# Optimization experiments

Hardware: AMD Instinct MI355X
Metric: run time of the kernel (lower is better)

Reference implementation:

```python
import math
import jax, jax.numpy as jnp
import numpy as np

VOCAB = 80; MAX_SEQ_LEN = 32; D_MODEL = 512; NHEAD = 8; DFF = 2048; NLAYERS = 6
EOS = 1; SOS = 2; PAD = 0; BATCH = 8; MEM_LEN = 256; PE_LEN = MAX_SEQ_LEN + 2
EPS = 1e-5


def _sinusoid(max_len, d):
    pos = np.arange(max_len)[:, None].astype(np.float32)
    div = np.exp(np.arange(0, d, 2).astype(np.float32) * -(math.log(10000.0) / d))
    pe = np.zeros((max_len, d), np.float32)
    pe[:, 0::2] = np.sin(pos * div)
    pe[:, 1::2] = np.cos(pos * div)
    return jnp.asarray(pe)


def setup_inputs() -> dict:
    key = jax.random.key(0)
    ks = jax.random.split(key, 10)
    s = 0.02
    def n(k, shape, scale=s):
        return jax.random.normal(k, shape, jnp.float32) * scale
    return {
        "memory": n(ks[0], (BATCH, MEM_LEN, D_MODEL), 1.0),
        "emb_table": n(ks[1], (VOCAB, D_MODEL), 1.0),
        "pe": _sinusoid(PE_LEN, D_MODEL),
        "sa_in_w": n(ks[2], (NLAYERS, 3 * D_MODEL, D_MODEL)),
        "sa_in_b": jnp.zeros((NLAYERS, 3 * D_MODEL), jnp.float32),
        "sa_out_w": n(ks[3], (NLAYERS, D_MODEL, D_MODEL)),
        "sa_out_b": jnp.zeros((NLAYERS, D_MODEL), jnp.float32),
        "ca_in_w": n(ks[4], (NLAYERS, 3 * D_MODEL, D_MODEL)),
        "ca_in_b": jnp.zeros((NLAYERS, 3 * D_MODEL), jnp.float32),
        "ca_out_w": n(ks[5], (NLAYERS, D_MODEL, D_MODEL)),
        "ca_out_b": jnp.zeros((NLAYERS, D_MODEL), jnp.float32),
        "ln_w": jnp.ones((NLAYERS, 3, D_MODEL), jnp.float32),
        "ln_b": jnp.zeros((NLAYERS, 3, D_MODEL), jnp.float32),
        "ff1_w": n(ks[6], (NLAYERS, DFF, D_MODEL)),
        "ff1_b": jnp.zeros((NLAYERS, DFF), jnp.float32),
        "ff2_w": n(ks[7], (NLAYERS, D_MODEL, DFF)),
        "ff2_b": jnp.zeros((NLAYERS, D_MODEL), jnp.float32),
        "clf_w": n(ks[8], (VOCAB, D_MODEL)),
        "clf_b": jnp.zeros((VOCAB,), jnp.float32),
    }


def _layer_norm(x, g, b):
    mu = jnp.mean(x, -1, keepdims=True)
    var = jnp.mean((x - mu) ** 2, -1, keepdims=True)
    return (x - mu) * jax.lax.rsqrt(var + EPS) * g + b


def _mha(q_in, kv_in, in_w, in_b, out_w, out_b, mask):
    d = q_in.shape[-1]; hd = d // NHEAD
    wq, wk, wv = jnp.split(in_w, 3, 0)
    bq, bk, bv = jnp.split(in_b, 3)
    B, Tq, _ = q_in.shape; Tk = kv_in.shape[1]
    q = (q_in @ wq.T + bq).reshape(B, Tq, NHEAD, hd)
    k = (kv_in @ wk.T + bk).reshape(B, Tk, NHEAD, hd)
    v = (kv_in @ wv.T + bv).reshape(B, Tk, NHEAD, hd)
    scores = jnp.einsum('bqhd,bkhd->bhqk', q, k) / math.sqrt(hd)
    if mask is not None:
        scores = jnp.where(mask, -1e9, scores)
    probs = jax.nn.softmax(scores, -1)
    out = jnp.einsum('bhqk,bkhd->bqhd', probs, v).reshape(B, Tq, d)
    return out @ out_w.T + out_b


def _decoder(tgt, memory, causal, p):
    # post-norm TransformerDecoder (torch default, dropout=identity at inference)
    x = tgt
    for l in range(NLAYERS):
        x = _layer_norm(x + _mha(x, x, p['sa_in_w'][l], p['sa_in_b'][l], p['sa_out_w'][l], p['sa_out_b'][l], causal), p['ln_w'][l, 0], p['ln_b'][l, 0])
        x = _layer_norm(x + _mha(x, memory, p['ca_in_w'][l], p['ca_in_b'][l], p['ca_out_w'][l], p['ca_out_b'][l], None), p['ln_w'][l, 1], p['ln_b'][l, 1])
        h = jax.nn.gelu(x @ p['ff1_w'][l].T + p['ff1_b'][l], approximate=False)
        x = _layer_norm(x + h @ p['ff2_w'][l].T + p['ff2_b'][l], p['ln_w'][l, 2], p['ln_b'][l, 2])
    return x


def _greedy(memory, emb_table, pe, p, clf_w, clf_b):
    B = memory.shape[0]; T1 = MAX_SEQ_LEN + 1
    sq = math.sqrt(D_MODEL)
    causal = jnp.triu(jnp.ones((T1, T1), bool), 1)[None, None]  # True = blocked
    tgt0 = jnp.zeros((B, T1, D_MODEL), memory.dtype)
    tgt0 = tgt0.at[:, 0].set(pe[0] + emb_table[SOS] * sq)

    def step(tgt, t):
        # full recompute of the whole decoder stack each step (no KV cache),
        # causal mask makes position t depend only on the valid prefix.
        out = _decoder(tgt, memory, causal, p)
        out_t = jax.lax.dynamic_slice_in_dim(out, t, 1, 1)[:, 0]
        logits = out_t @ clf_w.T + clf_b
        pred = jnp.argmax(logits, -1)
        # original uses pe[len(sampled_ids)] == pe[t+2] for the token at slot t+1
        new_e = jnp.take(pe, t + 2, axis=0) + emb_table[pred] * sq
        tgt = jax.lax.dynamic_update_slice_in_dim(tgt, new_e[:, None, :], t + 1, 1)
        return tgt, (logits, pred)

    _, (logits, preds) = jax.lax.scan(step, tgt0, jnp.arange(MAX_SEQ_LEN))
    all_logits = jnp.transpose(logits, (1, 0, 2))  # [B, T, V]
    sampled = jnp.concatenate([jnp.full((B, 1), SOS, preds.dtype), preds.T], 1)
    eos_idx = jnp.argmax(sampled == EOS, 1)  # first eos (0 if none, as torch)
    sampled = jnp.where(jnp.arange(T1)[None] <= eos_idx[:, None], PAD, sampled)
    return all_logits, sampled


def reference(memory, emb_table, pe, sa_in_w, sa_in_b, sa_out_w, sa_out_b, ca_in_w, ca_in_b, ca_out_w, ca_out_b, ln_w, ln_b, ff1_w, ff1_b, ff2_w, ff2_b, clf_w, clf_b):
    p = dict(sa_in_w=sa_in_w, sa_in_b=sa_in_b, sa_out_w=sa_out_w, sa_out_b=sa_out_b,
             ca_in_w=ca_in_w, ca_in_b=ca_in_b, ca_out_w=ca_out_w, ca_out_b=ca_out_b,
             ln_w=ln_w, ln_b=ln_b, ff1_w=ff1_w, ff1_b=ff1_b, ff2_w=ff2_w, ff2_b=ff2_b)
    return _greedy(memory, emb_table, pe, p, clf_w, clf_b)
```

## Files before the change

kernel.cpp:

```cpp
#include <hip/hip_runtime.h>
#include <math.h>

constexpr int T1 = 33, NL = 6, VOC = 80;
constexpr float SQD = 22.62741699796952f;

__device__ float g_memk[(size_t)NL * 2048 * 512];
__device__ float g_memv[(size_t)NL * 2048 * 512];
__device__ float g_kc[(size_t)NL * 8 * T1 * 512];
__device__ float g_vc[(size_t)NL * 8 * T1 * 512];
__device__ float g_x[8 * 512], g_x2[8 * 512], g_y[8 * 512], g_q[8 * 512], g_att[8 * 512];
__device__ float g_h[8 * 2048];
__device__ int   g_tok[8 * T1];

struct DecP {
  const float *mem, *emb, *pe, *saw, *sab, *sow, *sob, *caw, *cab, *cow, *cob,
              *lnw, *lnb, *f1w, *f1b, *f2w, *f2b, *cw, *cb;
  float* out;
};

__global__ __launch_bounds__(256) void k_memkv(const float* __restrict__ mem,
                                               const float* __restrict__ caw,
                                               const float* __restrict__ cab) {
  __shared__ float mlds[128][34];
  __shared__ float wlds[256][34];
  const int tid = threadIdx.x;
  const int l = blockIdx.x / 64, rem = blockIdx.x % 64;
  const int mt = rem >> 2, rt = rem & 3;
  const float* wbase = caw + (size_t)l * 1536 * 512 + (size_t)512 * 512;

  float acc[8][16];
#pragma unroll
  for (int i = 0; i < 8; ++i)
#pragma unroll
    for (int j = 0; j < 16; ++j) acc[i][j] = 0.f;

  const int tm = tid >> 4, tr = tid & 15;

  for (int kb = 0; kb < 16; ++kb) {
    __syncthreads();
    {
      int row = tid >> 1, half = tid & 1;
      const float2* src = (const float2*)(mem + (size_t)(mt * 128 + row) * 512 + kb * 32 + half * 16);
      float2* dst = (float2*)&mlds[row][half * 16];
#pragma unroll
      for (int q = 0; q < 8; ++q) dst[q] = src[q];
    }
    {
      int c2 = (tid & 15) * 2, rb = tid >> 4;
#pragma unroll
      for (int q = 0; q < 16; ++q) {
        int row = rb + 16 * q;
        *(float2*)&wlds[row][c2] =
            *(const float2*)(wbase + (size_t)(rt * 256 + row) * 512 + kb * 32 + c2);
      }
    }
    __syncthreads();
#pragma unroll 4
    for (int k2 = 0; k2 < 16; ++k2) {
      float2 mv[8];
#pragma unroll
      for (int i = 0; i < 8; ++i) mv[i] = *(const float2*)&mlds[tm * 8 + i][2 * k2];
#pragma unroll
      for (int j = 0; j < 16; ++j) {
        float2 w2 = *(const float2*)&wlds[tr + 16 * j][2 * k2];
#pragma unroll
        for (int i = 0; i < 8; ++i) acc[i][j] += mv[i].x * w2.x + mv[i].y * w2.y;
      }
    }
  }
#pragma unroll
  for (int i = 0; i < 8; ++i) {
    int mrow = mt * 128 + tm * 8 + i;
#pragma unroll
    for (int j = 0; j < 16; ++j) {
      int r = rt * 256 + tr + 16 * j;
      float v = acc[i][j] + cab[l * 1536 + 512 + r];
      if (r < 512) g_memk[((size_t)l * 2048 + mrow) * 512 + r] = v;
      else         g_memv[((size_t)l * 2048 + mrow) * 512 + (r - 512)] = v;
    }
  }
}

__device__ __forceinline__ float wave_reduce8(const float (&acc)[8], int lane) {
  float a0, a1, a2, a3;
  {
    bool hi = lane & 1;
    float s0 = hi ? acc[0] : acc[1], s1 = hi ? acc[2] : acc[3];
    float s2 = hi ? acc[4] : acc[5], s3 = hi ? acc[6] : acc[7];
    float r0 = __shfl_xor(s0, 1), r1 = __shfl_xor(s1, 1);
    float r2 = __shfl_xor(s2, 1), r3 = __shfl_xor(s3, 1);
    a0 = (hi ? acc[1] : acc[0]) + r0;  a1 = (hi ? acc[3] : acc[2]) + r1;
    a2 = (hi ? acc[5] : acc[4]) + r2;  a3 = (hi ? acc[7] : acc[6]) + r3;
  }
  float b0, b1;
  {
    bool hi = lane & 2;
    float s0 = hi ? a0 : a1, s1 = hi ? a2 : a3;
    float r0 = __shfl_xor(s0, 2), r1 = __shfl_xor(s1, 2);
    b0 = (hi ? a1 : a0) + r0;  b1 = (hi ? a3 : a2) + r1;
  }
  float f;
  {
    bool hi = lane & 4;
    float s = hi ? b0 : b1;
    float r = __shfl_xor(s, 4);
    f = (hi ? b1 : b0) + r;
  }
  f += __shfl_xor(f, 8);  f += __shfl_xor(f, 16);  f += __shfl_xor(f, 32);
  return f;
}

__device__ __forceinline__ void stage_in(float (*sx)[520], const float* __restrict__ g,
                                         bool doLN, const float* __restrict__ lw,
                                         const float* __restrict__ lb, float* __restrict__ wb) {
  const int tid = threadIdx.x;
#pragma unroll
  for (int q = 0; q < 4; ++q) {
    int f4 = tid + 256 * q;
    int b = f4 >> 7, c = (f4 & 127) << 2;
    float4 v = ((const float4*)g)[f4];
    *(float4*)&sx[b][c] = v;
  }
  __syncthreads();
  if (doLN) {
    const int lane = tid & 63, wv = tid >> 6;
#pragma unroll
    for (int rr = 0; rr < 2; ++rr) {
      int b = wv + 4 * rr;
      float vals[8]; float sm = 0.f;
#pragma unroll
      for (int j = 0; j < 8; ++j) { vals[j] = sx[b][lane + 64 * j]; sm += vals[j]; }
#pragma unroll
      for (int o = 32; o; o >>= 1) sm += __shfl_xor(sm, o);
      float mu = sm * (1.f / 512.f);
      float s2 = 0.f;
#pragma unroll
      for (int j = 0; j < 8; ++j) { float d = vals[j] - mu; s2 += d * d; }
#pragma unroll
      for (int o = 32; o; o >>= 1) s2 += __shfl_xor(s2, o);
      float rstd = 1.f / sqrtf(s2 * (1.f / 512.f) + 1e-5f);
#pragma unroll
      for (int j = 0; j < 8; ++j) {
        int c = lane + 64 * j;
        sx[b][c] = (vals[j] - mu) * rstd * lw[c] + lb[c];
      }
    }
    __syncthreads();
  }
  if (wb && blockIdx.x == 0) {
#pragma unroll
    for (int q = 0; q < 4; ++q) {
      int f4 = tid + 256 * q;
      int b = f4 >> 7, c = (f4 & 127) << 2;
      ((float4*)wb)[f4] = *(float4*)&sx[b][c];
    }
  }
}

template <int MODE>
__device__ __forceinline__ void gemv512(float (*sx)[520], const float* __restrict__ W,
                                        const float* __restrict__ bias, int rpb,
                                        float* __restrict__ out, const float* __restrict__ res,
                                        int l, int t) {
  const int lane = threadIdx.x & 63, wv = threadIdx.x >> 6;
  const int r0 = blockIdx.x * rpb;
  for (int rr = wv; rr < rpb; rr += 4) {
    const int r = r0 + rr;
    const float* wr = W + (size_t)r * 512;
    float acc[8] = {0, 0, 0, 0, 0, 0, 0, 0};
#pragma unroll
    for (int j = 0; j < 8; ++j) {
      float w = wr[lane + 64 * j];
#pragma unroll
      for (int b = 0; b < 8; ++b) acc[b] += w * sx[b][lane + 64 * j];
    }
    float f = wave_reduce8(acc, lane);
    if (lane < 8) {
      const int b = lane;
      float v = f + bias[r];
      if constexpr (MODE == 0) {
        if (r < 512)       out[b * 512 + r] = v;
        else if (r < 1024) g_kc[(((size_t)l * 8 + b) * T1 + t) * 512 + (r - 512)] = v;
        else               g_vc[(((size_t)l * 8 + b) * T1 + t) * 512 + (r - 1024)] = v;
      } else if constexpr (MODE == 1) {
        out[b * 512 + r] = v + res[b * 512 + r];
      } else if constexpr (MODE == 2) {
        out[b * 512 + r] = v;
      } else {
        out[b * 2048 + r] = 0.5f * v * (1.f + erff(v * 0.70710678118654752f));
      }
    }
  }
}

__device__ __forceinline__ void stage_h(float (*sb)[2052]) {
  const int tid = threadIdx.x;
#pragma unroll
  for (int q = 0; q < 16; ++q) {
    int f4 = tid + 256 * q;
    int b = f4 >> 9, c = (f4 & 511) << 2;
    *(float4*)&sb[b][c] = ((const float4*)g_h)[f4];
  }
}

__device__ __forceinline__ void gemvH(float (*sb)[2052], const float* __restrict__ W,
                                      const float* __restrict__ bias,
                                      const float* __restrict__ res, float* __restrict__ out) {
  const int lane = threadIdx.x & 63, wv = threadIdx.x >> 6;
  const int r0 = blockIdx.x * 8;
  for (int rr = wv; rr < 8; rr += 4) {
    const int r = r0 + rr;
    const float* wr = W + (size_t)r * 2048;
    float acc[8] = {0, 0, 0, 0, 0, 0, 0, 0};
#pragma unroll 8
    for (int j = 0; j < 32; ++j) {
      float w = wr[lane + 64 * j];
#pragma unroll
      for (int b = 0; b < 8; ++b) acc[b] += w * sb[b][lane + 64 * j];
    }
    float f = wave_reduce8(acc, lane);
    if (lane < 8) out[lane * 512 + r] = f + bias[r] + res[lane * 512 + r];
  }
}

__global__ __launch_bounds__(256) void k_start(DecP P) {
  int b = blockIdx.x;
#pragma unroll
  for (int q = 0; q < 2; ++q) {
    int c = threadIdx.x + 256 * q;
    g_x[b * 512 + c] = P.pe[c] + P.emb[2 * 512 + c] * SQD;
  }
  if (threadIdx.x == 0) g_tok[b * T1] = 2;
}

__global__ __launch_bounds__(256) void k_A(DecP P, int l, int t) {
  __shared__ float sx[8][520];
  const float* lw = (l > 0) ? P.lnw + ((l - 1) * 3 + 2) * 512 : P.lnw;
  const float* lb = (l > 0) ? P.lnb + ((l - 1) * 3 + 2) * 512 : P.lnb;
  stage_in(sx, (l == 0) ? g_x : g_y, l > 0, lw, lb, (l > 0) ? g_x : nullptr);
  gemv512<0>(sx, P.saw + (size_t)l * 1536 * 512, P.sab + l * 1536, 8, g_q, nullptr, l, t);
}

__global__ __launch_bounds__(64) void k_B(DecP P, int l, int t) {
  __shared__ float s_p[128];
  const int lane = threadIdx.x;
  const int b = blockIdx.x >> 3, h = blockIdx.x & 7;
  s_p[lane] = g_q[b * 512 + h * 64 + lane];
  asm volatile("s_waitcnt lgkmcnt(0)" ::: "memory");
  __builtin_amdgcn_sched_barrier(0);
  float sc = -3.4e38f;
  if (lane <= t) {
    const float4* kr = (const float4*)&g_kc[(((size_t)l * 8 + b) * T1 + lane) * 512 + h * 64];
    float s = 0.f;
#pragma unroll
    for (int d4 = 0; d4 < 16; ++d4) {
      float4 kv = kr[d4];
      s += s_p[d4 * 4 + 0] * kv.x + s_p[d4 * 4 + 1] * kv.y +
           s_p[d4 * 4 + 2] * kv.z + s_p[d4 * 4 + 3] * kv.w;
    }
    sc = s * 0.125f;
  }
  float m = sc;
#pragma unroll
  for (int o = 32; o; o >>= 1) m = fmaxf(m, __shfl_xor(m, o));
  float ex = (lane <= t) ? expf(sc - m) : 0.f;
  float sum = ex;
#pragma unroll
  for (int o = 32; o; o >>= 1) sum += __shfl_xor(sum, o);
  s_p[64 + lane] = ex / sum;
  asm volatile("s_waitcnt lgkmcnt(0)" ::: "memory");
  __builtin_amdgcn_sched_barrier(0);
  float o = 0.f;
  for (int j = 0; j <= t; ++j)
    o += s_p[64 + j] * g_vc[(((size_t)l * 8 + b) * T1 + j) * 512 + h * 64 + lane];
  g_att[b * 512 + h * 64 + lane] = o;
}

__global__ __launch_bounds__(256) void k_C(DecP P, int l) {
  __shared__ float sx[8][520];
  stage_in(sx, g_att, false, nullptr, nullptr, nullptr);
  gemv512<1>(sx, P.sow + (size_t)l * 512 * 512, P.sob + l * 512, 8, g_y, g_x, l, 0);
}

__global__ __launch_bounds__(256) void k_D(DecP P, int l) {
  __shared__ float sx[8][520];
  stage_in(sx, g_y, true, P.lnw + (l * 3 + 0) * 512, P.lnb + (l * 3 + 0) * 512, g_x2);
  gemv512<2>(sx, P.caw + (size_t)l * 1536 * 512, P.cab + l * 1536, 8, g_q, nullptr, l, 0);
}

__global__ __launch_bounds__(256) void k_E(DecP P, int l) {
  __shared__ float s_p[336];
  __shared__ float s_w[4][2];
  __shared__ float s_pv[4][64];
  const int tid = threadIdx.x;
  const int lane = tid & 63, wv = tid >> 6;
  const int b = blockIdx.x >> 3, h = blockIdx.x & 7;
  if (tid < 64) s_p[tid] = g_q[b * 512 + h * 64 + tid];
  __syncthreads();
  int m0 = wv * 64 + lane;
  const float4* kr = (const float4*)&g_memk[((size_t)l * 2048 + b * 256 + m0) * 512 + h * 64];
  float s = 0.f;
#pragma unroll
  for (int d4 = 0; d4 < 16; ++d4) {
    float4 kv = kr[d4];
    s += s_p[d4 * 4 + 0] * kv.x + s_p[d4 * 4 + 1] * kv.y +
         s_p[d4 * 4 + 2] * kv.z + s_p[d4 * 4 + 3] * kv.w;
  }
  s *= 0.125f;
  float m = s;
#pragma unroll
  for (int o = 32; o; o >>= 1) m = fmaxf(m, __shfl_xor(m, o));
  if (lane == 0) s_w[wv][0] = m;
  __syncthreads();
  float M = fmaxf(fmaxf(s_w[0][0], s_w[1][0]), fmaxf(s_w[2][0], s_w[3][0]));
  float ex = expf(s - M);
  float sum = ex;
#pragma unroll
  for (int o = 32; o; o >>= 1) sum += __shfl_xor(sum, o);
  if (lane == 0) s_w[wv][1] = sum;
  __syncthreads();
  float S = s_w[0][1] + s_w[1][1] + s_w[2][1] + s_w[3][1];
  s_p[64 + m0] = ex / S;
  __syncthreads();
  float o = 0.f;
  const float* vbase = &g_memv[((size_t)l * 2048 + b * 256) * 512 + h * 64];
  for (int j = 0; j < 64; ++j) {
    int mm = wv * 64 + j;
    o += s_p[64 + mm] * vbase[(size_t)mm * 512 + lane];
  }
  s_pv[wv][lane] = o;
  __syncthreads();
  if (wv == 0) {
    float tot = s_pv[0][lane] + s_pv[1][lane] + s_pv[2][lane] + s_pv[3][lane];
    g_att[b * 512 + h * 64 + lane] = tot;
  }
}

__global__ __launch_bounds__(256) void k_F(DecP P, int l) {
  __shared__ float sx[8][520];
  stage_in(sx, g_att, false, nullptr, nullptr, nullptr);
  gemv512<1>(sx, P.cow + (size_t)l * 512 * 512, P.cob + l * 512, 8, g_y, g_x2, l, 0);
}

__global__ __launch_bounds__(256) void k_G(DecP P, int l) {
  __shared__ float sx[8][520];
  stage_in(sx, g_y, true, P.lnw + (l * 3 + 1) * 512, P.lnb + (l * 3 + 1) * 512, g_x2);
  gemv512<3>(sx, P.f1w + (size_t)l * 2048 * 512, P.f1b + l * 2048, 8, g_h, nullptr, l, 0);
}

__global__ __launch_bounds__(256) void k_H(DecP P, int l) {
  __shared__ float sb[8][2052];
  stage_h(sb);
  __syncthreads();
  gemvH(sb, P.f2w + (size_t)l * 512 * 2048, P.f2b + l * 512, g_x2, g_y);
}

__global__ __launch_bounds__(256) void k_T(DecP P, int t) {
  __shared__ float sx[8][520];
  __shared__ float s_p[80];
  __shared__ int s_int[1];
  const int tid = threadIdx.x;
  const int lane = tid & 63, wv = tid >> 6;
  const int b = blockIdx.x;
  stage_in(sx, g_y, true, P.lnw + (5 * 3 + 2) * 512, P.lnb + (5 * 3 + 2) * 512, nullptr);
  for (int i = 0; i < 20; ++i) {
    int r = wv * 20 + i;
    const float* wr = P.cw + (size_t)r * 512;
    float a = 0.f;
#pragma unroll
    for (int j = 0; j < 8; ++j) a += wr[lane + 64 * j] * sx[b][lane + 64 * j];
#pragma unroll
    for (int o = 32; o; o >>= 1) a += __shfl_xor(a, o);
    if (lane == 0) {
      float v = a + P.cb[r];
      s_p[r] = v;
      P.out[((size_t)b * 32 + t) * VOC + r] = v;
    }
  }
  __syncthreads();
  if (wv == 0) {
    float v1 = s_p[lane];
    int i1 = lane;
    if (lane < 16) {
      float v2 = s_p[64 + lane];
      if (v2 > v1) { v1 = v2; i1 = 64 + lane; }
    }
#pragma unroll
    for (int o = 32; o; o >>= 1) {
      float ov = __shfl_xor(v1, o);
      int oi = __shfl_xor(i1, o);
      if (ov > v1 || (ov == v1 && oi < i1)) { v1 = ov; i1 = oi; }
    }
    if (lane == 0) { s_int[0] = i1; g_tok[b * T1 + t + 1] = i1; }
  }
  __syncthreads();
  int pred = s_int[0];
#pragma unroll
  for (int q = 0; q < 2; ++q) {
    int c = tid + 256 * q;
    g_x[b * 512 + c] = P.pe[(t + 2) * 512 + c] + P.emb[(size_t)pred * 512 + c] * SQD;
  }
}

__global__ __launch_bounds__(64) void k_out(DecP P) {
  int lane = threadIdx.x;
  if (lane < 8) {
    int b = lane;
    int eos = -1;
    for (int j = 0; j < T1; ++j) {
      int tk = g_tok[b * T1 + j];
      if (tk == 1 && eos < 0) eos = j;
    }
    if (eos < 0) eos = 0;
    for (int j = 0; j < T1; ++j) {
      int tk = g_tok[b * T1 + j];
      P.out[20480 + b * T1 + j] = (j <= eos) ? 0.f : (float)tk;
    }
  }
}

extern "C" void kernel_launch(void* const* d_in, const int* in_sizes, int n_in,
                              void* d_out, int out_size, void* d_ws, size_t ws_size,
                              hipStream_t stream) {
  (void)in_sizes; (void)n_in; (void)d_ws; (void)ws_size; (void)out_size;
  const float* mem = (const float*)d_in[0];
  const float* emb = (const float*)d_in[1];
  const float* pe  = (const float*)d_in[2];
  const float* saw = (const float*)d_in[3];
  const float* sab = (const float*)d_in[4];
  const float* sow = (const float*)d_in[5];
  const float* sob = (const float*)d_in[6];
  const float* caw = (const float*)d_in[7];
  const float* cab = (const float*)d_in[8];
  const float* cow = (const float*)d_in[9];
  const float* cob = (const float*)d_in[10];
  const float* lnw = (const float*)d_in[11];
  const float* lnb = (const float*)d_in[12];
  const float* f1w = (const float*)d_in[13];
  const float* f1b = (const float*)d_in[14];
  const float* f2w = (const float*)d_in[15];
  const float* f2b = (const float*)d_in[16];
  const float* cw  = (const float*)d_in[17];
  const float* cb  = (const float*)d_in[18];

  DecP P{mem, emb, pe, saw, sab, sow, sob, caw, cab, cow, cob,
         lnw, lnb, f1w, f1b, f2w, f2b, cw, cb, (float*)d_out};

  hipLaunchKernelGGL(k_start, dim3(8), dim3(256), 0, stream, P);
  hipLaunchKernelGGL(k_memkv, dim3(384), dim3(256), 0, stream, mem, caw, cab);

  for (int t = 0; t < 32; ++t) {
    for (int l = 0; l < NL; ++l) {
      hipLaunchKernelGGL(k_A, dim3(192), dim3(256), 0, stream, P, l, t);
      hipLaunchKernelGGL(k_B, dim3(64), dim3(64), 0, stream, P, l, t);
      hipLaunchKernelGGL(k_C, dim3(64), dim3(256), 0, stream, P, l);
      hipLaunchKernelGGL(k_D, dim3(64), dim3(256), 0, stream, P, l);
      hipLaunchKernelGGL(k_E, dim3(64), dim3(256), 0, stream, P, l);
      hipLaunchKernelGGL(k_F, dim3(64), dim3(256), 0, stream, P, l);
      hipLaunchKernelGGL(k_G, dim3(256), dim3(256), 0, stream, P, l);
      hipLaunchKernelGGL(k_H, dim3(64), dim3(256), 0, stream, P, l);
    }
    hipLaunchKernelGGL(k_T, dim3(8), dim3(256), 0, stream, P, t);
  }
  hipLaunchKernelGGL(k_out, dim3(1), dim3(64), 0, stream, P);
}
```

Before: 8.999 ms.

## Prefetch weight rows into registers before staging activations, one row per wave

Each GEMV kernel now runs 512 threads (8 waves), and each wave owns exactly one weight row. It issues that row's global loads into registers before staging and layer-normalising the activations into LDS. The intent is to overlap the weight fetch latency with the activation staging, the LayerNorm and the barrier, instead of serialising them. The FF2 kernel holds 32 weight values per lane in registers. This raises register pressure and changes the per-block work split.

```diff
diff --git a/kernel.cpp b/kernel.cpp
--- a/kernel.cpp
+++ b/kernel.cpp
@@ -110,47 +110,48 @@
   return f;
 }
 
-__device__ __forceinline__ void stage_in(float (*sx)[520], const float* __restrict__ g,
+__device__ __forceinline__ void keep8(const float (&w)[8]) {
+  asm volatile("" :: "v"(w[0]), "v"(w[1]), "v"(w[2]), "v"(w[3]),
+                     "v"(w[4]), "v"(w[5]), "v"(w[6]), "v"(w[7]));
+}
+
+__device__ __forceinline__ void stage512(float (*sx)[520], const float* __restrict__ g,
                                          bool doLN, const float* __restrict__ lw,
                                          const float* __restrict__ lb, float* __restrict__ wb) {
   const int tid = threadIdx.x;
 #pragma unroll
-  for (int q = 0; q < 4; ++q) {
-    int f4 = tid + 256 * q;
+  for (int q = 0; q < 2; ++q) {
+    int f4 = tid + 512 * q;
     int b = f4 >> 7, c = (f4 & 127) << 2;
     float4 v = ((const float4*)g)[f4];
     *(float4*)&sx[b][c] = v;
   }
   __syncthreads();
   if (doLN) {
-    const int lane = tid & 63, wv = tid >> 6;
-#pragma unroll
-    for (int rr = 0; rr < 2; ++rr) {
-      int b = wv + 4 * rr;
-      float vals[8]; float sm = 0.f;
-#pragma unroll
-      for (int j = 0; j < 8; ++j) { vals[j] = sx[b][lane + 64 * j]; sm += vals[j]; }
-#pragma unroll
-      for (int o = 32; o; o >>= 1) sm += __shfl_xor(sm, o);
-      float mu = sm * (1.f / 512.f);
-      float s2 = 0.f;
-#pragma unroll
-      for (int j = 0; j < 8; ++j) { float d = vals[j] - mu; s2 += d * d; }
-#pragma unroll
-      for (int o = 32; o; o >>= 1) s2 += __shfl_xor(s2, o);
-      float rstd = 1.f / sqrtf(s2 * (1.f / 512.f) + 1e-5f);
-#pragma unroll
-      for (int j = 0; j < 8; ++j) {
-        int c = lane + 64 * j;
-        sx[b][c] = (vals[j] - mu) * rstd * lw[c] + lb[c];
-      }
+    const int lane = tid & 63, b = tid >> 6;
+    float vals[8]; float sm = 0.f;
+#pragma unroll
+    for (int j = 0; j < 8; ++j) { vals[j] = sx[b][lane + 64 * j]; sm += vals[j]; }
+#pragma unroll
+    for (int o = 32; o; o >>= 1) sm += __shfl_xor(sm, o);
+    float mu = sm * (1.f / 512.f);
+    float s2 = 0.f;
+#pragma unroll
+    for (int j = 0; j < 8; ++j) { float d = vals[j] - mu; s2 += d * d; }
+#pragma unroll
+    for (int o = 32; o; o >>= 1) s2 += __shfl_xor(s2, o);
+    float rstd = 1.f / sqrtf(s2 * (1.f / 512.f) + 1e-5f);
+#pragma unroll
+    for (int j = 0; j < 8; ++j) {
+      int c = lane + 64 * j;
+      sx[b][c] = (vals[j] - mu) * rstd * lw[c] + lb[c];
     }
     __syncthreads();
   }
   if (wb && blockIdx.x == 0) {
 #pragma unroll
-    for (int q = 0; q < 4; ++q) {
-      int f4 = tid + 256 * q;
+    for (int q = 0; q < 2; ++q) {
+      int f4 = tid + 512 * q;
       int b = f4 >> 7, c = (f4 & 127) << 2;
       ((float4*)wb)[f4] = *(float4*)&sx[b][c];
     }
@@ -158,68 +159,32 @@
 }
 
 template <int MODE>
-__device__ __forceinline__ void gemv512(float (*sx)[520], const float* __restrict__ W,
-                                        const float* __restrict__ bias, int rpb,
+__device__ __forceinline__ void gemv_pf(float (*sx)[520], const float (&w)[8], int r,
+                                        const float* __restrict__ bias,
                                         float* __restrict__ out, const float* __restrict__ res,
                                         int l, int t) {
-  const int lane = threadIdx.x & 63, wv = threadIdx.x >> 6;
-  const int r0 = blockIdx.x * rpb;
-  for (int rr = wv; rr < rpb; rr += 4) {
-    const int r = r0 + rr;
-    const float* wr = W + (size_t)r * 512;
-    float acc[8] = {0, 0, 0, 0, 0, 0, 0, 0};
-#pragma unroll
-    for (int j = 0; j < 8; ++j) {
-      float w = wr[lane + 64 * j];
-#pragma unroll
-      for (int b = 0; b < 8; ++b) acc[b] += w * sx[b][lane + 64 * j];
-    }
-    float f = wave_reduce8(acc, lane);
-    if (lane < 8) {
-      const int b = lane;
-      float v = f + bias[r];
-      if constexpr (MODE == 0) {
-        if (r < 512)       out[b * 512 + r] = v;
-        else if (r < 1024) g_kc[(((size_t)l * 8 + b) * T1 + t) * 512 + (r - 512)] = v;
-        else               g_vc[(((size_t)l * 8 + b) * T1 + t) * 512 + (r - 1024)] = v;
-      } else if constexpr (MODE == 1) {
-        out[b * 512 + r] = v + res[b * 512 + r];
-      } else if constexpr (MODE == 2) {
-        out[b * 512 + r] = v;
-      } else {
-        out[b * 2048 + r] = 0.5f * v * (1.f + erff(v * 0.70710678118654752f));
-      }
-    }
-  }
-}
-
-__device__ __forceinline__ void stage_h(float (*sb)[2052]) {
-  const int tid = threadIdx.x;
-#pragma unroll
-  for (int q = 0; q < 16; ++q) {
-    int f4 = tid + 256 * q;
-    int b = f4 >> 9, c = (f4 & 511) << 2;
-    *(float4*)&sb[b][c] = ((const float4*)g_h)[f4];
-  }
-}
-
-__device__ __forceinline__ void gemvH(float (*sb)[2052], const float* __restrict__ W,
-                                      const float* __restrict__ bias,
-                                      const float* __restrict__ res, float* __restrict__ out) {
-  const int lane = threadIdx.x & 63, wv = threadIdx.x >> 6;
-  const int r0 = blockIdx.x * 8;
-  for (int rr = wv; rr < 8; rr += 4) {
-    const int r = r0 + rr;
-    const float* wr = W + (size_t)r * 2048;
-    float acc[8] = {0, 0, 0, 0, 0, 0, 0, 0};
-#pragma unroll 8
-    for (int j = 0; j < 32; ++j) {
-      float w = wr[lane + 64 * j];
-#pragma unroll
-      for (int b = 0; b < 8; ++b) acc[b] += w * sb[b][lane + 64 * j];
-    }
-    float f = wave_reduce8(acc, lane);
-    if (lane < 8) out[lane * 512 + r] = f + bias[r] + res[lane * 512 + r];
+  const int lane = threadIdx.x & 63;
+  float acc[8] = {0, 0, 0, 0, 0, 0, 0, 0};
+#pragma unroll
+  for (int j = 0; j < 8; ++j) {
+#pragma unroll
+    for (int b = 0; b < 8; ++b) acc[b] += w[j] * sx[b][lane + 64 * j];
+  }
+  float f = wave_reduce8(acc, lane);
+  if (lane < 8) {
+    const int b = lane;
+    float v = f + bias[r];
+    if constexpr (MODE == 0) {
+      if (r < 512)       out[b * 512 + r] = v;
+      else if (r < 1024) g_kc[(((size_t)l * 8 + b) * T1 + t) * 512 + (r - 512)] = v;
+      else               g_vc[(((size_t)l * 8 + b) * T1 + t) * 512 + (r - 1024)] = v;
+    } else if constexpr (MODE == 1) {
+      out[b * 512 + r] = v + res[b * 512 + r];
+    } else if constexpr (MODE == 2) {
+      out[b * 512 + r] = v;
+    } else {
+      out[b * 2048 + r] = 0.5f * v * (1.f + erff(v * 0.70710678118654752f));
+    }
   }
 }
 
@@ -233,12 +198,19 @@
   if (threadIdx.x == 0) g_tok[b * T1] = 2;
 }
 
-__global__ __launch_bounds__(256) void k_A(DecP P, int l, int t) {
+__global__ __launch_bounds__(512) void k_A(DecP P, int l, int t) {
   __shared__ float sx[8][520];
+  const int lane = threadIdx.x & 63, wv = threadIdx.x >> 6;
+  const int r = blockIdx.x * 8 + wv;
+  const float* wr = P.saw + (size_t)l * 1536 * 512 + (size_t)r * 512;
+  float w[8];
+#pragma unroll
+  for (int j = 0; j < 8; ++j) w[j] = wr[lane + 64 * j];
+  keep8(w);
   const float* lw = (l > 0) ? P.lnw + ((l - 1) * 3 + 2) * 512 : P.lnw;
   const float* lb = (l > 0) ? P.lnb + ((l - 1) * 3 + 2) * 512 : P.lnb;
-  stage_in(sx, (l == 0) ? g_x : g_y, l > 0, lw, lb, (l > 0) ? g_x : nullptr);
-  gemv512<0>(sx, P.saw + (size_t)l * 1536 * 512, P.sab + l * 1536, 8, g_q, nullptr, l, t);
+  stage512(sx, (l == 0) ? g_x : g_y, l > 0, lw, lb, (l > 0) ? g_x : nullptr);
+  gemv_pf<0>(sx, w, r, P.sab + l * 1536, g_q, nullptr, l, t);
 }
 
 __global__ __launch_bounds__(64) void k_B(DecP P, int l, int t) {
@@ -276,16 +248,30 @@
   g_att[b * 512 + h * 64 + lane] = o;
 }
 
-__global__ __launch_bounds__(256) void k_C(DecP P, int l) {
+__global__ __launch_bounds__(512) void k_C(DecP P, int l) {
   __shared__ float sx[8][520];
-  stage_in(sx, g_att, false, nullptr, nullptr, nullptr);
-  gemv512<1>(sx, P.sow + (size_t)l * 512 * 512, P.sob + l * 512, 8, g_y, g_x, l, 0);
-}
-
-__global__ __launch_bounds__(256) void k_D(DecP P, int l) {
+  const int lane = threadIdx.x & 63, wv = threadIdx.x >> 6;
+  const int r = blockIdx.x * 8 + wv;
+  const float* wr = P.sow + (size_t)l * 512 * 512 + (size_t)r * 512;
+  float w[8];
+#pragma unroll
+  for (int j = 0; j < 8; ++j) w[j] = wr[lane + 64 * j];
+  keep8(w);
+  stage512(sx, g_att, false, nullptr, nullptr, nullptr);
+  gemv_pf<1>(sx, w, r, P.sob + l * 512, g_y, g_x, l, 0);
+}
+
+__global__ __launch_bounds__(512) void k_D(DecP P, int l) {
   __shared__ float sx[8][520];
-  stage_in(sx, g_y, true, P.lnw + (l * 3 + 0) * 512, P.lnb + (l * 3 + 0) * 512, g_x2);
-  gemv512<2>(sx, P.caw + (size_t)l * 1536 * 512, P.cab + l * 1536, 8, g_q, nullptr, l, 0);
+  const int lane = threadIdx.x & 63, wv = threadIdx.x >> 6;
+  const int r = blockIdx.x * 8 + wv;
+  const float* wr = P.caw + (size_t)l * 1536 * 512 + (size_t)r * 512;
+  float w[8];
+#pragma unroll
+  for (int j = 0; j < 8; ++j) w[j] = wr[lane + 64 * j];
+  keep8(w);
+  stage512(sx, g_y, true, P.lnw + (l * 3 + 0) * 512, P.lnb + (l * 3 + 0) * 512, g_x2);
+  gemv_pf<2>(sx, w, r, P.cab + l * 1536, g_q, nullptr, l, 0);
 }
 
 __global__ __launch_bounds__(256) void k_E(DecP P, int l) {
@@ -336,35 +322,89 @@
   }
 }
 
-__global__ __launch_bounds__(256) void k_F(DecP P, int l) {
+__global__ __launch_bounds__(512) void k_F(DecP P, int l) {
   __shared__ float sx[8][520];
-  stage_in(sx, g_att, false, nullptr, nullptr, nullptr);
-  gemv512<1>(sx, P.cow + (size_t)l * 512 * 512, P.cob + l * 512, 8, g_y, g_x2, l, 0);
-}
-
-__global__ __launch_bounds__(256) void k_G(DecP P, int l) {
+  const int lane = threadIdx.x & 63, wv = threadIdx.x >> 6;
+  const int r = blockIdx.x * 8 + wv;
+  const float* wr = P.cow + (size_t)l * 512 * 512 + (size_t)r * 512;
+  float w[8];
+#pragma unroll
+  for (int j = 0; j < 8; ++j) w[j] = wr[lane + 64 * j];
+  keep8(w);
+  stage512(sx, g_att, false, nullptr, nullptr, nullptr);
+  gemv_pf<1>(sx, w, r, P.cob + l * 512, g_y, g_x2, l, 0);
+}
+
+__global__ __launch_bounds__(512) void k_G(DecP P, int l) {
   __shared__ float sx[8][520];
-  stage_in(sx, g_y, true, P.lnw + (l * 3 + 1) * 512, P.lnb + (l * 3 + 1) * 512, g_x2);
-  gemv512<3>(sx, P.f1w + (size_t)l * 2048 * 512, P.f1b + l * 2048, 8, g_h, nullptr, l, 0);
-}
-
-__global__ __launch_bounds__(256) void k_H(DecP P, int l) {
+  const int lane = threadIdx.x & 63, wv = threadIdx.x >> 6;
+  const int r = blockIdx.x * 8 + wv;
+  const float* wr = P.f1w + (size_t)l * 2048 * 512 + (size_t)r * 512;
+  float w[8];
+#pragma unroll
+  for (int j = 0; j < 8; ++j) w[j] = wr[lane + 64 * j];
+  keep8(w);
+  stage512(sx, g_y, true, P.lnw + (l * 3 + 1) * 512, P.lnb + (l * 3 + 1) * 512, g_x2);
+  gemv_pf<3>(sx, w, r, P.f1b + l * 2048, g_h, nullptr, l, 0);
+}
+
+__global__ __launch_bounds__(512) void k_H(DecP P, int l) {
   __shared__ float sb[8][2052];
-  stage_h(sb);
-  __syncthreads();
-  gemvH(sb, P.f2w + (size_t)l * 512 * 2048, P.f2b + l * 512, g_x2, g_y);
-}
-
-__global__ __launch_bounds__(256) void k_T(DecP P, int t) {
+  const int tid = threadIdx.x;
+  const int lane = tid & 63, wv = tid >> 6;
+  const int r = blockIdx.x * 8 + wv;
+  const float* wr = P.f2w + (size_t)l * 512 * 2048 + (size_t)r * 2048;
+  float w0[8], w1[8], w2[8], w3[8];
+#pragma unroll
+  for (int j = 0; j < 8; ++j) {
+    w0[j] = wr[lane + 64 * j];
+    w1[j] = wr[lane + 64 * (j + 8)];
+    w2[j] = wr[lane + 64 * (j + 16)];
+    w3[j] = wr[lane + 64 * (j + 24)];
+  }
+  keep8(w0); keep8(w1); keep8(w2); keep8(w3);
+#pragma unroll
+  for (int q = 0; q < 8; ++q) {
+    int f4 = tid + 512 * q;
+    int b = f4 >> 9, c = (f4 & 511) << 2;
+    *(float4*)&sb[b][c] = ((const float4*)g_h)[f4];
+  }
+  __syncthreads();
+  float acc[8] = {0, 0, 0, 0, 0, 0, 0, 0};
+#pragma unroll
+  for (int j = 0; j < 8; ++j) {
+#pragma unroll
+    for (int b = 0; b < 8; ++b) acc[b] += w0[j] * sb[b][lane + 64 * j];
+  }
+#pragma unroll
+  for (int j = 0; j < 8; ++j) {
+#pragma unroll
+    for (int b = 0; b < 8; ++b) acc[b] += w1[j] * sb[b][lane + 64 * (j + 8)];
+  }
+#pragma unroll
+  for (int j = 0; j < 8; ++j) {
+#pragma unroll
+    for (int b = 0; b < 8; ++b) acc[b] += w2[j] * sb[b][lane + 64 * (j + 16)];
+  }
+#pragma unroll
+  for (int j = 0; j < 8; ++j) {
+#pragma unroll
+    for (int b = 0; b < 8; ++b) acc[b] += w3[j] * sb[b][lane + 64 * (j + 24)];
+  }
+  float f = wave_reduce8(acc, lane);
+  if (lane < 8) g_y[lane * 512 + r] = f + P.f2b[l * 512 + r] + g_x2[lane * 512 + r];
+}
+
+__global__ __launch_bounds__(512) void k_T(DecP P, int t) {
   __shared__ float sx[8][520];
   __shared__ float s_p[80];
   __shared__ int s_int[1];
   const int tid = threadIdx.x;
   const int lane = tid & 63, wv = tid >> 6;
   const int b = blockIdx.x;
-  stage_in(sx, g_y, true, P.lnw + (5 * 3 + 2) * 512, P.lnb + (5 * 3 + 2) * 512, nullptr);
-  for (int i = 0; i < 20; ++i) {
-    int r = wv * 20 + i;
+  stage512(sx, g_y, true, P.lnw + (5 * 3 + 2) * 512, P.lnb + (5 * 3 + 2) * 512, nullptr);
+  for (int i = 0; i < 10; ++i) {
+    int r = wv * 10 + i;
     const float* wr = P.cw + (size_t)r * 512;
     float a = 0.f;
 #pragma unroll
@@ -395,9 +435,8 @@
   }
   __syncthreads();
   int pred = s_int[0];
-#pragma unroll
-  for (int q = 0; q < 2; ++q) {
-    int c = tid + 256 * q;
+  {
+    int c = tid;
     g_x[b * 512 + c] = P.pe[(t + 2) * 512 + c] + P.emb[(size_t)pred * 512 + c] * SQD;
   }
 }
@@ -451,16 +490,16 @@
 
   for (int t = 0; t < 32; ++t) {
     for (int l = 0; l < NL; ++l) {
-      hipLaunchKernelGGL(k_A, dim3(192), dim3(256), 0, stream, P, l, t);
+      hipLaunchKernelGGL(k_A, dim3(192), dim3(512), 0, stream, P, l, t);
       hipLaunchKernelGGL(k_B, dim3(64), dim3(64), 0, stream, P, l, t);
-      hipLaunchKernelGGL(k_C, dim3(64), dim3(256), 0, stream, P, l);
-      hipLaunchKernelGGL(k_D, dim3(64), dim3(256), 0, stream, P, l);
+      hipLaunchKernelGGL(k_C, dim3(64), dim3(512), 0, stream, P, l);
+      hipLaunchKernelGGL(k_D, dim3(64), dim3(512), 0, stream, P, l);
       hipLaunchKernelGGL(k_E, dim3(64), dim3(256), 0, stream, P, l);
-      hipLaunchKernelGGL(k_F, dim3(64), dim3(256), 0, stream, P, l);
-      hipLaunchKernelGGL(k_G, dim3(256), dim3(256), 0, stream, P, l);
-      hipLaunchKernelGGL(k_H, dim3(64), dim3(256), 0, stream, P, l);
-    }
-    hipLaunchKernelGGL(k_T, dim3(8), dim3(256), 0, stream, P, t);
+      hipLaunchKernelGGL(k_F, dim3(64), dim3(512), 0, stream, P, l);
+      hipLaunchKernelGGL(k_G, dim3(256), dim3(512), 0, stream, P, l);
+      hipLaunchKernelGGL(k_H, dim3(64), dim3(512), 0, stream, P, l);
+    }
+    hipLaunchKernelGGL(k_T, dim3(8), dim3(512), 0, stream, P, t);
   }
   hipLaunchKernelGGL(k_out, dim3(1), dim3(64), 0, stream, P);
 }
```

Result: faster. 8.023 ms (-10.8%).
